# Optimization experiments

Hardware: AMD Instinct MI355X
Metric: run time of the kernel (lower is better)

The kernel has to match this reference:

```python
import jax, jax.numpy as jnp
import numpy as np

HID = 2048; NH = 16; DQN = 128; DR = 64; DV = 128; QLR = 1536; KVLR = 512
DQ = DQN + DR  # 192
S = 2048; B = 2
EPS = 1e-6; BASE = 10000.0


def rmsnorm(x, w, eps=EPS):
    xf = x.astype(jnp.float32)
    v = jnp.mean(jnp.square(xf), axis=-1, keepdims=True)
    return (xf * jax.lax.rsqrt(v + eps)).astype(x.dtype) * w


def rope_cos_sin(seq_len, dim):
    inv_freq = 1.0 / (BASE ** (jnp.arange(0, dim, 2, dtype=jnp.float32) / dim))
    freqs = jnp.outer(jnp.arange(seq_len, dtype=jnp.float32), inv_freq)  # [s, d/2]
    emb = jnp.concatenate([freqs, freqs], axis=-1)  # [s, d]
    return jnp.cos(emb), jnp.sin(emb)


def rotate_half(x):
    x1, x2 = jnp.split(x, 2, axis=-1)
    return jnp.concatenate([-x2, x1], axis=-1)


def apply_rope(q, k, cos, sin, position_ids):
    # DeepSeek-V2 variant: interleaved-pair reorder before rotate_half
    cos = cos[position_ids][:, None]  # [b,1,s,d]
    sin = sin[position_ids][:, None]

    def deinterleave(x):
        b, h, s, d = x.shape
        return x.reshape(b, h, s, d // 2, 2).transpose(0, 1, 2, 4, 3).reshape(b, h, s, d)

    q = deinterleave(q)
    k = deinterleave(k)
    return q * cos + rotate_half(q) * sin, k * cos + rotate_half(k) * sin


def setup_inputs() -> dict:
    key = jax.random.key(0)
    ks = jax.random.split(key, 8)
    hidden_states = jax.random.normal(ks[0], (S, B, HID), dtype=jnp.float32)
    causal = jnp.tril(jnp.ones((S, S), dtype=bool))
    attention_mask = jnp.where(causal, 0.0, -1e9).astype(jnp.float32)
    attention_mask = jnp.broadcast_to(attention_mask[None, None], (B, 1, S, S)) + 0.0
    position_ids = jnp.broadcast_to(jnp.arange(S, dtype=jnp.int64 if jax.config.jax_enable_x64 else jnp.int32), (B, S)) + 0
    w = 0.02
    wq_a = jax.random.normal(ks[1], (QLR, HID), dtype=jnp.float32) * w
    q_a_ln_w = jnp.ones((QLR,), dtype=jnp.float32)
    wq_b = jax.random.normal(ks[2], (NH * DQ, QLR), dtype=jnp.float32) * w
    wkv_a = jax.random.normal(ks[3], (KVLR + DR, HID), dtype=jnp.float32) * w
    kv_a_ln_w = jnp.ones((KVLR,), dtype=jnp.float32)
    wkv_b = jax.random.normal(ks[4], (NH * (DQN + DV), KVLR), dtype=jnp.float32) * w
    wo = jax.random.normal(ks[5], (HID, NH * DV), dtype=jnp.float32) * w
    return {"hidden_states": hidden_states, "attention_mask": attention_mask,
            "position_ids": position_ids, "wq_a": wq_a, "q_a_ln_w": q_a_ln_w,
            "wq_b": wq_b, "wkv_a": wkv_a, "kv_a_ln_w": kv_a_ln_w,
            "wkv_b": wkv_b, "wo": wo}


def reference(hidden_states, attention_mask, position_ids, wq_a, q_a_ln_w, wq_b,
              wkv_a, kv_a_ln_w, wkv_b, wo):
    s, b, _ = hidden_states.shape
    # low-rank Q projection: a -> RMSNorm -> b
    q = hidden_states @ wq_a.T                      # [s,b,QLR]
    q = rmsnorm(q, q_a_ln_w) @ wq_b.T               # [s,b,NH*DQ]
    q = q.reshape(s, b, NH, DQ).transpose(1, 2, 0, 3)  # [b,h,s,dq]
    q_nope, q_pe = q[..., :DQN], q[..., DQN:]
    # joint compressed KV + shared rope key
    ckv = hidden_states @ wkv_a.T                   # [s,b,KVLR+DR]
    compressed_kv, k_pe = ckv[..., :KVLR], ckv[..., KVLR:]
    k_pe = k_pe.reshape(s, b, 1, DR).transpose(1, 2, 0, 3)  # [b,1,s,dr]
    kv = rmsnorm(compressed_kv, kv_a_ln_w) @ wkv_b.T         # [s,b,NH*(DQN+DV)]
    kv = kv.reshape(s, b, NH, DQN + DV).transpose(1, 2, 0, 3)
    k_nope, v = kv[..., :DQN], kv[..., DQN:]
    # partial-dim RoPE
    cos, sin = rope_cos_sin(s, DR)
    q_pe, k_pe = apply_rope(q_pe, k_pe, cos, sin, position_ids)
    query = jnp.concatenate([q_nope, q_pe], axis=-1)                 # [b,h,s,dq]
    key = jnp.concatenate([k_nope, jnp.broadcast_to(k_pe, (b, NH, s, DR))], axis=-1)
    scale = DQ ** -0.5
    scores = jnp.einsum('bhqd,bhkd->bhqk', query, key) * scale + attention_mask
    attn = jax.nn.softmax(scores.astype(jnp.float32), axis=-1).astype(query.dtype)
    out = jnp.einsum('bhqk,bhkd->bhqd', attn, v)    # [b,h,s,dv]
    out = out.transpose(2, 0, 1, 3).reshape(s, b, NH * DV)
    return out @ wo.T                               # [s,b,HID]
```

## Files before the change

### kernel.cpp

```cpp
#include <hip/hip_runtime.h>
#include <cmath>

typedef unsigned short u16;
typedef __bf16 bf16x8 __attribute__((ext_vector_type(8)));
typedef float f32x4 __attribute__((ext_vector_type(4)));

#define MFMA16(a,b,c) __builtin_amdgcn_mfma_f32_16x16x32_bf16((a),(b),(c),0,0,0)

__device__ __forceinline__ u16 f2bf(float f){
  union { float f; unsigned u; } x; x.f = f;
  unsigned r = x.u + 0x7FFFu + ((x.u >> 16) & 1u);
  return (u16)(r >> 16);
}
__device__ __forceinline__ float bf2f(u16 v){
  union { unsigned u; float f; } x; x.u = ((unsigned)v) << 16; return x.f;
}
__device__ __forceinline__ void gload16(const void* g, void* l){
  __builtin_amdgcn_global_load_lds((const __attribute__((address_space(1))) void*)g,
                                   (__attribute__((address_space(3))) void*)l, 16, 0, 0);
}
__device__ __forceinline__ float block_sum256(float v, float* red, int tid){
  #pragma unroll
  for (int off = 32; off; off >>= 1) v += __shfl_xor(v, off);
  if ((tid & 63) == 0) red[tid >> 6] = v;
  __syncthreads();
  return red[0] + red[1] + red[2] + red[3];
}

__global__ __launch_bounds__(256) void k_conv(const float* __restrict__ in,
                                              u16* __restrict__ out, int n4){
  int i = blockIdx.x * 256 + threadIdx.x;
  int stride = gridDim.x * 256;
  for (; i < n4; i += stride){
    float4 v = reinterpret_cast<const float4*>(in)[i];
    ushort4 o; o.x = f2bf(v.x); o.y = f2bf(v.y); o.z = f2bf(v.z); o.w = f2bf(v.w);
    reinterpret_cast<ushort4*>(out)[i] = o;
  }
}

__global__ __launch_bounds__(256) void k_convw(const float* __restrict__ s0,
                                               const float* __restrict__ s1,
                                               const float* __restrict__ s2,
                                               const float* __restrict__ s3,
                                               u16* __restrict__ d0, u16* __restrict__ d1,
                                               u16* __restrict__ d2, u16* __restrict__ d3){
  const int n0 = 1536 * 2048 / 4, n1 = 3072 * 1536 / 4;
  const int n2 = 4096 * 512 / 4,  n3 = 2048 * 2048 / 4;
  const int total = n0 + n1 + n2 + n3;
  int i = blockIdx.x * 256 + threadIdx.x;
  int stride = gridDim.x * 256;
  for (; i < total; i += stride){
    const float* s; u16* d; int j = i;
    if (j < n0){ s = s0; d = d0; }
    else if ((j -= n0) < n1){ s = s1; d = d1; }
    else if ((j -= n1) < n2){ s = s2; d = d2; }
    else { j -= n2; s = s3; d = d3; }
    float4 v = reinterpret_cast<const float4*>(s)[j];
    ushort4 o; o.x = f2bf(v.x); o.y = f2bf(v.y); o.z = f2bf(v.z); o.w = f2bf(v.w);
    reinterpret_cast<ushort4*>(d)[j] = o;
  }
}

__global__ __launch_bounds__(256) void k_conv_kva(const float* __restrict__ in,
                                                  u16* __restrict__ out){
  const int n4 = 640 * 2048 / 4;
  int i = blockIdx.x * 256 + threadIdx.x;
  int stride = gridDim.x * 256;
  for (; i < n4; i += stride){
    int e = i * 4; int row = e >> 11; int col = e & 2047;
    ushort4 o;
    if (row < 576){
      float4 v = *reinterpret_cast<const float4*>(in + (size_t)row * 2048 + col);
      o.x = f2bf(v.x); o.y = f2bf(v.y); o.z = f2bf(v.z); o.w = f2bf(v.w);
    } else { o.x = 0; o.y = 0; o.z = 0; o.w = 0; }
    reinterpret_cast<ushort4*>(out)[i] = o;
  }
}

template<int OUT_BF16>
__global__ __launch_bounds__(256) void k_gemm(const u16* __restrict__ A,
                                              const u16* __restrict__ Bm,
                                              void* __restrict__ Cv,
                                              int M, int N, int K){
  __shared__ __align__(16) u16 sA[128 * 32];
  __shared__ __align__(16) u16 sB[128 * 32];
  const int tid = threadIdx.x, w = tid >> 6, l = tid & 63;
  const int ln = l & 15, lg = l >> 4;
  const int m0 = blockIdx.x * 128, n0 = blockIdx.y * 128;
  const int wr = w >> 1, wc = w & 1;
  const int trow = tid >> 2, tcol = (tid & 3) * 8;

  const f32x4 zf = {0.f, 0.f, 0.f, 0.f};
  f32x4 acc[4][4];
  #pragma unroll
  for (int i = 0; i < 4; ++i)
    #pragma unroll
    for (int j = 0; j < 4; ++j) acc[i][j] = zf;

  const u16* ga = A  + (size_t)(m0 + trow) * K + tcol;
  const u16* gb = Bm + (size_t)(n0 + trow) * K + tcol;
  char* la = (char*)sA + w * 1024;
  char* lb = (char*)sB + w * 1024;
  const int nk = K >> 5;

  for (int kt = 0; kt < nk; ++kt){
    __syncthreads();
    gload16(ga,                 la);
    gload16(ga + (size_t)64 * K, la + 4096);
    gload16(gb,                 lb);
    gload16(gb + (size_t)64 * K, lb + 4096);
    ga += 32; gb += 32;
    __syncthreads();

    bf16x8 af[4], bfr[4];
    #pragma unroll
    for (int i = 0; i < 4; ++i)
      af[i] = *(const bf16x8*)&sA[(wr * 64 + i * 16 + ln) * 32 + lg * 8];
    #pragma unroll
    for (int j = 0; j < 4; ++j)
      bfr[j] = *(const bf16x8*)&sB[(wc * 64 + j * 16 + ln) * 32 + lg * 8];
    #pragma unroll
    for (int i = 0; i < 4; ++i)
      #pragma unroll
      for (int j = 0; j < 4; ++j)
        acc[i][j] = MFMA16(af[i], bfr[j], acc[i][j]);
  }

  const int mb = m0 + wr * 64, nb = n0 + wc * 64;
  #pragma unroll
  for (int i = 0; i < 4; ++i)
    #pragma unroll
    for (int j = 0; j < 4; ++j)
      #pragma unroll
      for (int r = 0; r < 4; ++r){
        int mm = mb + i * 16 + lg * 4 + r;
        int nn = nb + j * 16 + ln;
        if (OUT_BF16) ((u16*)Cv)[(size_t)mm * N + nn] = f2bf(acc[i][j][r]);
        else          ((float*)Cv)[(size_t)mm * N + nn] = acc[i][j][r];
      }
}

__global__ __launch_bounds__(256) void k_rms_fused(const float* __restrict__ in,
                                                   const float* __restrict__ wq,
                                                   const float* __restrict__ wkv,
                                                   u16* __restrict__ outq,
                                                   u16* __restrict__ outkv,
                                                   u16* __restrict__ kpe){
  __shared__ float red[4];
  const int row = blockIdx.x, tid = threadIdx.x;
  const float* x = in + (size_t)row * 2176;
  float ss = 0.f;
  #pragma unroll
  for (int i = tid; i < 1536; i += 256){ float v = x[i]; ss += v * v; }
  float tot = block_sum256(ss, red, tid);
  float inv = rsqrtf(tot * (1.f / 1536.f) + 1e-6f);
  #pragma unroll
  for (int i = tid; i < 1536; i += 256)
    outq[(size_t)row * 1536 + i] = f2bf(x[i] * inv * wq[i]);
  __syncthreads();
  const float* y = x + 1536;
  float v0 = y[tid], v1 = y[tid + 256];
  float tot2 = block_sum256(v0 * v0 + v1 * v1, red, tid);
  float inv2 = rsqrtf(tot2 * (1.f / 512.f) + 1e-6f);
  outkv[(size_t)row * 512 + tid]       = f2bf(v0 * inv2 * wkv[tid]);
  outkv[(size_t)row * 512 + tid + 256] = f2bf(v1 * inv2 * wkv[tid + 256]);
  if (tid < 32){
    int j = tid;
    float e = y[512 + 2 * j], o = y[512 + 2 * j + 1];
    float pos  = (float)(row >> 1);
    float invf = exp2f(-13.287712379549449f * (float)j * (1.f / 32.f));
    float th = pos * invf, sn = sinf(th), cs = cosf(th);
    kpe[(size_t)row * 64 + j]      = f2bf(e * cs - o * sn);
    kpe[(size_t)row * 64 + 32 + j] = f2bf(o * cs + e * sn);
  }
}

__global__ __launch_bounds__(64) void k_rope_q(const u16* __restrict__ q,
                                               u16* __restrict__ qpe){
  const int sb = blockIdx.x;
  const int h  = blockIdx.y * 2 + (threadIdx.x >> 5);
  const int j  = threadIdx.x & 31;
  const u16* base = q + (size_t)sb * 3072 + h * 192 + 128;
  float e = bf2f(base[2 * j]), o = bf2f(base[2 * j + 1]);
  float pos  = (float)(sb >> 1);
  float invf = exp2f(-13.287712379549449f * (float)j * (1.f / 32.f));
  float th = pos * invf, sn = sinf(th), cs = cosf(th);
  u16* dst = qpe + ((size_t)sb * 16 + h) * 64;
  dst[j]      = f2bf(e * cs - o * sn);
  dst[32 + j] = f2bf(o * cs + e * sn);
}

__global__ __launch_bounds__(256) void k_vtrans(const u16* __restrict__ kv,
                                                u16* __restrict__ vt){
  __shared__ u16 t[64][65];
  const int bh = blockIdx.z, b = bh >> 4, h = bh & 15;
  const int s0 = blockIdx.x * 64, d0 = blockIdx.y * 64;
  const int tid = threadIdx.x;
  #pragma unroll
  for (int i = 0; i < 16; ++i){
    int idx = i * 256 + tid; int si = idx >> 6, di = idx & 63;
    t[si][di] = kv[(size_t)((s0 + si) * 2 + b) * 4096 + h * 256 + 128 + d0 + di];
  }
  __syncthreads();
  #pragma unroll
  for (int i = 0; i < 16; ++i){
    int idx = i * 256 + tid; int di = idx >> 6, si = idx & 63;
    vt[(size_t)((b * 16 + h) * 128 + d0 + di) * 2048 + s0 + si] = t[si][di];
  }
}

__global__ __launch_bounds__(256, 2) void k_attn(const u16* __restrict__ q,
                                                 const u16* __restrict__ qpe,
                                                 const u16* __restrict__ kv,
                                                 const u16* __restrict__ kpe,
                                                 const u16* __restrict__ vt,
                                                 u16* __restrict__ out){
  const int i_ = blockIdx.x + 16 * (blockIdx.y + 16 * blockIdx.z);
  const int j_ = i_ >> 3, x_ = i_ & 7;
  const int g_ = x_ * 4 + (j_ >> 4);
  const int bx = j_ & 15;
  const int h = g_ & 15, b = g_ >> 4;
  const int bh = b * 16 + h;
  const int tid = threadIdx.x, w = tid >> 6, l = tid & 63;
  const int ln = l & 15, lg = l >> 4;

  __shared__ __align__(16) u16 sK[2][64 * 128];
  __shared__ __align__(16) u16 sPE[2][64 * 64];
  __shared__ __align__(16) u16 sV[2][128 * 64];

  const f32x4 zf = {0.f, 0.f, 0.f, 0.f};
  const float SCL2 = 0.104117549f;

  #define PERM(pr_) ((((pr_) >> 5) << 5) + ((((pr_) >> 2) & 3) << 3) + \
                     ((((pr_) >> 4) & 1) << 2) + ((pr_) & 3))
  #define STAGE(kt_, bi_) {                                                     \
    _Pragma("unroll")                                                           \
    for (int p = 0; p < 4; ++p){                                                \
      int o_ = p * 4096 + tid * 16;                                             \
      int pr = o_ >> 8, cl = (o_ >> 4) & 15, cg = cl ^ (pr & 7);                \
      int kl = PERM(pr);                                                        \
      gload16(kv + (size_t)(((kt_) * 64 + kl) * 2 + b) * 4096 + h * 256 + cg * 8, \
              (char*)sK[bi_] + o_);                                             \
    }                                                                           \
    _Pragma("unroll")                                                           \
    for (int p = 0; p < 2; ++p){                                                \
      int o_ = p * 4096 + tid * 16;                                             \
      int pr = o_ >> 7, cl = (o_ >> 4) & 7, cg = cl ^ (pr & 7);                 \
      int kl = PERM(pr);                                                        \
      gload16(kpe + (size_t)(((kt_) * 64 + kl) * 2 + b) * 64 + cg * 8,          \
              (char*)sPE[bi_] + o_);                                            \
    }                                                                           \
    _Pragma("unroll")                                                           \
    for (int p = 0; p < 4; ++p){                                                \
      int o_ = p * 4096 + tid * 16;                                             \
      int row = o_ >> 7, cl = (o_ >> 4) & 7, cg = cl ^ (row & 7);               \
      gload16(vt + (size_t)(bh * 128 + row) * 2048 + (kt_) * 64 + cg * 8,       \
              (char*)sV[bi_] + o_);                                             \
    } }

  for (int half = 0; half < 2; ++half){
    const int qt = half ? (31 - bx) : bx;
    const int qrow0 = qt * 64 + w * 16;
    const int sq = qrow0 + ln;

    bf16x8 qf[6];
    {
      const u16* qr = q + (size_t)(sq * 2 + b) * 3072 + h * 192;
      #pragma unroll
      for (int kb = 0; kb < 4; ++kb) qf[kb] = *(const bf16x8*)(qr + kb * 32 + lg * 8);
      const u16* pr_ = qpe + ((size_t)(sq * 2 + b) * 16 + h) * 64;
      qf[4] = *(const bf16x8*)(pr_ + lg * 8);
      qf[5] = *(const bf16x8*)(pr_ + 32 + lg * 8);
    }

    f32x4 o[8];
    float m_i = -3.0e38f, l_i = 0.f;
    #pragma unroll
    for (int c8 = 0; c8 < 8; ++c8) o[c8] = zf;

    const int nkt = qt + 1;
    STAGE(0, 0);
    __syncthreads();

    for (int kt = 0; kt < nkt; ++kt){
      const int bi = kt & 1;
      if (kt + 1 < nkt) STAGE(kt + 1, bi ^ 1);

      f32x4 s_[4];
      #pragma unroll
      for (int cb = 0; cb < 4; ++cb){
        int rl = cb * 16 + ln, swz = rl & 7;
        bf16x8 kf[6];
        #pragma unroll
        for (int kb = 0; kb < 4; ++kb)
          kf[kb] = *(const bf16x8*)((char*)sK[bi] + rl * 256 + (((kb * 4 + lg) ^ swz) << 4));
        kf[4] = *(const bf16x8*)((char*)sPE[bi] + rl * 128 + ((lg ^ swz) << 4));
        kf[5] = *(const bf16x8*)((char*)sPE[bi] + rl * 128 + (((4 + lg) ^ swz) << 4));
        f32x4 acc = zf;
        #pragma unroll
        for (int kb = 0; kb < 6; ++kb)
          acc = MFMA16(kf[kb], qf[kb], acc);
        s_[cb] = acc;
      }

      const bool needMask = (kt * 64 + 63) > qrow0;
      float mx = -3.0e38f;
      #pragma unroll
      for (int cb = 0; cb < 4; ++cb)
        #pragma unroll
        for (int r = 0; r < 4; ++r){
          float v = s_[cb][r] * SCL2;
          if (needMask){
            int sk = kt * 64 + 32 * (cb >> 1) + 8 * lg + 4 * (cb & 1) + r;
            v = (sk <= sq) ? v : -3.0e38f;
          }
          s_[cb][r] = v;
          mx = fmaxf(mx, v);
        }
      mx = fmaxf(mx, __shfl_xor(mx, 16));
      mx = fmaxf(mx, __shfl_xor(mx, 32));
      if (!__all(mx <= m_i + 11.6f)){
        float mn = fmaxf(m_i, mx);
        float sf = exp2f(m_i - mn);
        m_i = mn;
        l_i *= sf;
        float sf0 = __shfl(sf, 4 * lg + 0);
        float sf1 = __shfl(sf, 4 * lg + 1);
        float sf2 = __shfl(sf, 4 * lg + 2);
        float sf3 = __shfl(sf, 4 * lg + 3);
        #pragma unroll
        for (int c8 = 0; c8 < 8; ++c8){
          o[c8][0] *= sf0; o[c8][1] *= sf1; o[c8][2] *= sf2; o[c8][3] *= sf3;
        }
      }
      float rs = 0.f;
      #pragma unroll
      for (int cb = 0; cb < 4; ++cb)
        #pragma unroll
        for (int r = 0; r < 4; ++r){
          float p = exp2f(s_[cb][r] - m_i);
          s_[cb][r] = p;
          rs += p;
        }
      rs += __shfl_xor(rs, 16);
      rs += __shfl_xor(rs, 32);
      l_i += rs;

      bf16x8 pa[2];
      #pragma unroll
      for (int hf = 0; hf < 2; ++hf){
        unsigned pw0, pw1, pw2, pw3;
        f32x4 sa = s_[hf * 2], sb2 = s_[hf * 2 + 1];
        asm("v_cvt_pk_bf16_f32 %0, %1, %2" : "=v"(pw0) : "v"(sa[0]),  "v"(sa[1]));
        asm("v_cvt_pk_bf16_f32 %0, %1, %2" : "=v"(pw1) : "v"(sa[2]),  "v"(sa[3]));
        asm("v_cvt_pk_bf16_f32 %0, %1, %2" : "=v"(pw2) : "v"(sb2[0]), "v"(sb2[1]));
        asm("v_cvt_pk_bf16_f32 %0, %1, %2" : "=v"(pw3) : "v"(sb2[2]), "v"(sb2[3]));
        union { uint4 u; bf16x8 v; } pk;
        pk.u.x = pw0; pk.u.y = pw1; pk.u.z = pw2; pk.u.w = pw3;
        pa[hf] = pk.v;
      }

      #pragma unroll
      for (int c8 = 0; c8 < 8; ++c8){
        int d = c8 * 16 + ln, swz = d & 7;
        bf16x8 vf0 = *(const bf16x8*)((char*)sV[bi] + d * 128 + ((lg ^ swz) << 4));
        bf16x8 vf1 = *(const bf16x8*)((char*)sV[bi] + d * 128 + (((4 + lg) ^ swz) << 4));
        o[c8] = MFMA16(pa[0], vf0, o[c8]);
        o[c8] = MFMA16(pa[1], vf1, o[c8]);
      }
      __syncthreads();
    }

    float li0 = __shfl(l_i, 4 * lg + 0);
    float li1 = __shfl(l_i, 4 * lg + 1);
    float li2 = __shfl(l_i, 4 * lg + 2);
    float li3 = __shfl(l_i, 4 * lg + 3);
    float iv0 = 1.f / li0, iv1 = 1.f / li1, iv2 = 1.f / li2, iv3 = 1.f / li3;
    int sqr = qrow0 + lg * 4;
    #pragma unroll
    for (int c8 = 0; c8 < 8; ++c8){
      int col = h * 128 + c8 * 16 + ln;
      out[(size_t)((sqr + 0) * 2 + b) * 2048 + col] = f2bf(o[c8][0] * iv0);
      out[(size_t)((sqr + 1) * 2 + b) * 2048 + col] = f2bf(o[c8][1] * iv1);
      out[(size_t)((sqr + 2) * 2 + b) * 2048 + col] = f2bf(o[c8][2] * iv2);
      out[(size_t)((sqr + 3) * 2 + b) * 2048 + col] = f2bf(o[c8][3] * iv3);
    }
  }
  #undef STAGE
  #undef PERM
}

extern "C" void kernel_launch(void* const* d_in, const int* in_sizes, int n_in,
                              void* d_out, int out_size, void* d_ws, size_t ws_size,
                              hipStream_t stream){
  const float* hidden    = (const float*)d_in[0];
  const float* wq_a      = (const float*)d_in[3];
  const float* q_a_ln_w  = (const float*)d_in[4];
  const float* wq_b      = (const float*)d_in[5];
  const float* wkv_a     = (const float*)d_in[6];
  const float* kv_a_ln_w = (const float*)d_in[7];
  const float* wkv_b     = (const float*)d_in[8];
  const float* wo        = (const float*)d_in[9];

  char* ws = (char*)d_ws;
  size_t off = 0;
  auto alloc = [&](size_t bytes){ size_t o = off; off += (bytes + 255) & ~(size_t)255; return o; };
  const size_t SB = 4096;

  u16*   hid_bf   = (u16*)(ws + alloc(SB * 2048 * 2));
  u16*   wqab_bf  = (u16*)(ws + alloc((size_t)2176 * 2048 * 2));
  u16*   wqb_bf   = (u16*)(ws + alloc((size_t)3072 * 1536 * 2));
  u16*   wkvb_bf  = (u16*)(ws + alloc((size_t)4096 * 512 * 2));
  u16*   wo_bf    = (u16*)(ws + alloc((size_t)2048 * 2048 * 2));
  float* qa_f     = (float*)(ws + alloc(SB * 2176 * 4));
  u16*   qrms_bf  = (u16*)(ws + alloc(SB * 1536 * 2));
  u16*   ckvr_bf  = (u16*)(ws + alloc(SB * 512 * 2));
  u16*   kpe_bf   = (u16*)(ws + alloc(SB * 64 * 2));
  u16*   qfull_bf = (u16*)(ws + alloc(SB * 3072 * 2));
  u16*   qpe_bf   = (u16*)(ws + alloc(SB * 16 * 64 * 2));
  u16*   kv_bf    = (u16*)(ws + alloc(SB * 4096 * 2));
  u16*   vt_bf    = hid_bf;
  u16*   attn_bf  = (u16*)qa_f;

  dim3 blk(256);
  k_conv<<<2048, blk, 0, stream>>>(hidden, hid_bf, (int)(SB * 2048 / 4));
  k_convw<<<2048, blk, 0, stream>>>(wq_a, wq_b, wkv_b, wo,
                                    wqab_bf, wqb_bf, wkvb_bf, wo_bf);
  k_conv_kva<<<512, blk, 0, stream>>>(wkv_a, wqab_bf + (size_t)1536 * 2048);
  k_gemm<0><<<dim3(32, 17), blk, 0, stream>>>(hid_bf, wqab_bf, qa_f, 4096, 2176, 2048);
  k_rms_fused<<<4096, blk, 0, stream>>>(qa_f, q_a_ln_w, kv_a_ln_w, qrms_bf, ckvr_bf, kpe_bf);
  k_gemm<1><<<dim3(32, 24), blk, 0, stream>>>(qrms_bf, wqb_bf, qfull_bf, 4096, 3072, 1536);
  k_rope_q<<<dim3(4096, 8), dim3(64), 0, stream>>>(qfull_bf, qpe_bf);
  k_gemm<1><<<dim3(32, 32), blk, 0, stream>>>(ckvr_bf, wkvb_bf, kv_bf, 4096, 4096, 512);
  k_vtrans<<<dim3(32, 2, 32), blk, 0, stream>>>(kv_bf, vt_bf);
  k_attn<<<dim3(16, 16, 2), blk, 0, stream>>>(qfull_bf, qpe_bf, kv_bf, kpe_bf, vt_bf, attn_bf);
  k_gemm<0><<<dim3(32, 16), blk, 0, stream>>>(attn_bf, wo_bf, d_out, 4096, 2048, 2048);
}
```

Before: 342.3 us.

## Double-buffer GEMM LDS loads, swizzle workgroup order, fold softmax scale into wq_b

```diff
diff --git a/kernel.cpp b/kernel.cpp
--- a/kernel.cpp
+++ b/kernel.cpp
@@ -47,16 +47,18 @@
   const int n0 = 1536 * 2048 / 4, n1 = 3072 * 1536 / 4;
   const int n2 = 4096 * 512 / 4,  n3 = 2048 * 2048 / 4;
   const int total = n0 + n1 + n2 + n3;
+  const float SCL2 = 0.104117549f;
   int i = blockIdx.x * 256 + threadIdx.x;
   int stride = gridDim.x * 256;
   for (; i < total; i += stride){
-    const float* s; u16* d; int j = i;
+    const float* s; u16* d; int j = i; float m = 1.f;
     if (j < n0){ s = s0; d = d0; }
-    else if ((j -= n0) < n1){ s = s1; d = d1; }
+    else if ((j -= n0) < n1){ s = s1; d = d1; m = SCL2; }
     else if ((j -= n1) < n2){ s = s2; d = d2; }
     else { j -= n2; s = s3; d = d3; }
     float4 v = reinterpret_cast<const float4*>(s)[j];
-    ushort4 o; o.x = f2bf(v.x); o.y = f2bf(v.y); o.z = f2bf(v.z); o.w = f2bf(v.w);
+    ushort4 o; o.x = f2bf(v.x * m); o.y = f2bf(v.y * m);
+    o.z = f2bf(v.z * m); o.w = f2bf(v.w * m);
     reinterpret_cast<ushort4*>(d)[j] = o;
   }
 }
@@ -82,11 +84,16 @@
                                               const u16* __restrict__ Bm,
                                               void* __restrict__ Cv,
                                               int M, int N, int K){
-  __shared__ __align__(16) u16 sA[128 * 32];
-  __shared__ __align__(16) u16 sB[128 * 32];
+  __shared__ __align__(16) u16 sA[2][128 * 32];
+  __shared__ __align__(16) u16 sB[2][128 * 32];
   const int tid = threadIdx.x, w = tid >> 6, l = tid & 63;
   const int ln = l & 15, lg = l >> 4;
-  const int m0 = blockIdx.x * 128, n0 = blockIdx.y * 128;
+  const int id  = blockIdx.x + gridDim.x * blockIdx.y;
+  const int nwg = gridDim.x * gridDim.y;
+  const int swz = (id & 7) * (nwg >> 3) + (id >> 3);
+  const int bx  = swz & (gridDim.x - 1);
+  const int by  = swz / gridDim.x;
+  const int m0 = bx * 128, n0 = by * 128;
   const int wr = w >> 1, wc = w & 1;
   const int trow = tid >> 2, tcol = (tid & 3) * 8;
 
@@ -99,32 +106,40 @@
 
   const u16* ga = A  + (size_t)(m0 + trow) * K + tcol;
   const u16* gb = Bm + (size_t)(n0 + trow) * K + tcol;
-  char* la = (char*)sA + w * 1024;
-  char* lb = (char*)sB + w * 1024;
   const int nk = K >> 5;
 
+  #define GSTAGE(kt_, bi_) {                                   \
+    char* la_ = (char*)sA[bi_] + w * 1024;                     \
+    char* lb_ = (char*)sB[bi_] + w * 1024;                     \
+    gload16(ga + (kt_) * 32,                  la_);            \
+    gload16(ga + (kt_) * 32 + (size_t)64 * K, la_ + 4096);     \
+    gload16(gb + (kt_) * 32,                  lb_);            \
+    gload16(gb + (kt_) * 32 + (size_t)64 * K, lb_ + 4096);     \
+  }
+
+  GSTAGE(0, 0);
+  __syncthreads();
+
   for (int kt = 0; kt < nk; ++kt){
-    __syncthreads();
-    gload16(ga,                 la);
-    gload16(ga + (size_t)64 * K, la + 4096);
-    gload16(gb,                 lb);
-    gload16(gb + (size_t)64 * K, lb + 4096);
-    ga += 32; gb += 32;
-    __syncthreads();
+    const int bi = kt & 1;
+    if (kt + 1 < nk) GSTAGE(kt + 1, bi ^ 1);
 
     bf16x8 af[4], bfr[4];
     #pragma unroll
     for (int i = 0; i < 4; ++i)
-      af[i] = *(const bf16x8*)&sA[(wr * 64 + i * 16 + ln) * 32 + lg * 8];
+      af[i] = *(const bf16x8*)&sA[bi][(wr * 64 + i * 16 + ln) * 32 + lg * 8];
     #pragma unroll
     for (int j = 0; j < 4; ++j)
-      bfr[j] = *(const bf16x8*)&sB[(wc * 64 + j * 16 + ln) * 32 + lg * 8];
+      bfr[j] = *(const bf16x8*)&sB[bi][(wc * 64 + j * 16 + ln) * 32 + lg * 8];
     #pragma unroll
     for (int i = 0; i < 4; ++i)
       #pragma unroll
       for (int j = 0; j < 4; ++j)
         acc[i][j] = MFMA16(af[i], bfr[j], acc[i][j]);
-  }
+
+    __syncthreads();
+  }
+  #undef GSTAGE
 
   const int mb = m0 + wr * 64, nb = n0 + wc * 64;
   #pragma unroll
@@ -229,7 +244,6 @@
   __shared__ __align__(16) u16 sV[2][128 * 64];
 
   const f32x4 zf = {0.f, 0.f, 0.f, 0.f};
-  const float SCL2 = 0.104117549f;
 
   #define PERM(pr_) ((((pr_) >> 5) << 5) + ((((pr_) >> 2) & 3) << 3) + \
                      ((((pr_) >> 4) & 1) << 2) + ((pr_) & 3))
@@ -309,7 +323,7 @@
       for (int cb = 0; cb < 4; ++cb)
         #pragma unroll
         for (int r = 0; r < 4; ++r){
-          float v = s_[cb][r] * SCL2;
+          float v = s_[cb][r];
           if (needMask){
             int sk = kt * 64 + 32 * (cb >> 1) + 8 * lg + 4 * (cb & 1) + r;
             v = (sk <= sq) ? v : -3.0e38f;
```

Result: faster. 313.5 us (-8.4%).
